# Performance work log

Measured on AMD Instinct MI355X. Metric: run time of the kernel, lower is better.

## Reference

```python
import jax, jax.numpy as jnp
import numpy as np

B, T, E, H = 2, 2048, 1024, 16


def setup_inputs() -> dict:
    key = jax.random.key(0)
    ks = jax.random.split(key, 6)
    s = lambda k, shape: jax.random.normal(k, shape, dtype=jnp.float32) * 0.02
    return {
        "x": jax.random.normal(ks[0], (B, T, E), dtype=jnp.float32),
        "ln1_g": jnp.ones((E,), jnp.float32),
        "ln1_b": jnp.zeros((E,), jnp.float32),
        "attn_w": s(ks[1], (E, 3 * E)),
        "attn_b": jnp.zeros((3 * E,), jnp.float32),
        "proj_w": s(ks[2], (E, E)),
        "proj_b": jnp.zeros((E,), jnp.float32),
        "ln2_g": jnp.ones((E,), jnp.float32),
        "ln2_b": jnp.zeros((E,), jnp.float32),
        "mlp_w1": s(ks[3], (E, 4 * E)),
        "mlp_b1": jnp.zeros((4 * E,), jnp.float32),
        "mlp_w2": s(ks[4], (4 * E, E)),
        "mlp_b2": jnp.zeros((E,), jnp.float32),
        "w_att": jnp.ones((1,), jnp.float32),
        "w_mlp": jnp.ones((1,), jnp.float32),
    }


def _ln(x, g, b, eps=1e-5):
    m = x.mean(-1, keepdims=True)
    v = ((x - m) ** 2).mean(-1, keepdims=True)
    return (x - m) * jax.lax.rsqrt(v + eps) * g + b


def reference(x, ln1_g, ln1_b, attn_w, attn_b, proj_w, proj_b,
              ln2_g, ln2_b, mlp_w1, mlp_b1, mlp_w2, mlp_b2, w_att, w_mlp):
    Bx, Tx, Ex = x.shape
    hd = Ex // H
    # --- self-attention on ln_1(x) ---
    qkv = _ln(x, ln1_g, ln1_b) @ attn_w + attn_b          # [B,T,3E]
    q, k, v = jnp.split(qkv, 3, axis=-1)
    q = q.reshape(Bx, Tx, H, hd)
    k = k.reshape(Bx, Tx, H, hd)
    v = v.reshape(Bx, Tx, H, hd)
    att = jnp.einsum('bthd,bshd->bhts', q, k) * (1.0 / np.sqrt(hd))  # [B,H,T,T]
    causal = jnp.tril(jnp.ones((Tx, Tx), dtype=bool))
    att = jnp.where(causal, att, -jnp.inf)
    att = jax.nn.softmax(att, axis=-1)
    y = jnp.einsum('bhts,bshd->bthd', att, v).reshape(Bx, Tx, Ex)
    y = y @ proj_w + proj_b
    x = x * w_att + y
    # --- MLP on ln_2(x) ---
    h = _ln(x, ln2_g, ln2_b) @ mlp_w1 + mlp_b1
    h = jax.nn.gelu(h, approximate=False)
    x = x * w_mlp + (h @ mlp_w2 + mlp_b2)
    return x
```

## Files before the change

### kernel.cpp

```cpp
#include <hip/hip_runtime.h>
#include <math.h>

typedef __bf16 bf16;
typedef bf16 bf16x8 __attribute__((ext_vector_type(8)));
typedef bf16 bf16x4 __attribute__((ext_vector_type(4)));
typedef float f32x4 __attribute__((ext_vector_type(4)));

#define MFMA(a, b, c) __builtin_amdgcn_mfma_f32_16x16x32_bf16((a), (b), (c), 0, 0, 0)

#define GLOAD_LDS16(gp, lp)                                                        \
  __builtin_amdgcn_global_load_lds((const __attribute__((address_space(1))) void*)(gp), \
                                   (__attribute__((address_space(3))) void*)(lp), 16, 0, 0)

static const size_t E_WT_ATTN = 0;
static const size_t E_WT_PROJ = 3145728;
static const size_t E_WT_MLP1 = 4194304;
static const size_t E_WT_MLP2 = 8388608;
static const size_t E_LN1     = 12582912;
static const size_t E_QKV     = 16777216;
static const size_t E_VT      = 37748736;
static const size_t E_Y       = 41943040;
static const size_t E_LN2     = 46137344;
static const size_t E_H       = 50331648;
static const size_t BYTE_X2    = 134217728;
static const size_t BYTE_OPART = 150994944;
static const size_t BYTE_ML    = 184549376;
static const size_t BYTE_GPART = 185597952;
static const size_t TOTAL_BYTES = 252706816;

__device__ __align__(4096) unsigned char g_buf[TOTAL_BYTES];

__global__ __launch_bounds__(256) void transpose_all(const float* __restrict__ aw,
                                                     const float* __restrict__ pw,
                                                     const float* __restrict__ m1,
                                                     const float* __restrict__ m2,
                                                     bf16* __restrict__ o_a,
                                                     bf16* __restrict__ o_p,
                                                     bf16* __restrict__ o_m1,
                                                     bf16* __restrict__ o_m2) {
  __shared__ float tile[32][33];
  int bid = blockIdx.x;
  const float* in;
  bf16* out;
  int K, N, tix;
  if (bid < 3072) { in = aw; out = o_a; K = 1024; N = 3072; tix = bid; }
  else if (bid < 4096) { in = pw; out = o_p; K = 1024; N = 1024; tix = bid - 3072; }
  else if (bid < 8192) { in = m1; out = o_m1; K = 1024; N = 4096; tix = bid - 4096; }
  else { in = m2; out = o_m2; K = 4096; N = 1024; tix = bid - 8192; }
  int ntx = N >> 5;
  int bx = tix % ntx, by = tix / ntx;
  int tx = threadIdx.x, ty = threadIdx.y;
#pragma unroll
  for (int i = ty; i < 32; i += 8)
    tile[i][tx] = in[(size_t)(by * 32 + i) * N + bx * 32 + tx];
  __syncthreads();
#pragma unroll
  for (int i = ty; i < 32; i += 8)
    out[(size_t)(bx * 32 + i) * K + by * 32 + tx] = (bf16)tile[tx][i];
}

__global__ __launch_bounds__(256) void ln_bf16(const float* __restrict__ x,
                                               const float* __restrict__ g,
                                               const float* __restrict__ b,
                                               bf16* __restrict__ out) {
  int row = blockIdx.x, tid = threadIdx.x;
  const float* xr = x + ((size_t)row << 10);
  float4 v = *(const float4*)(xr + tid * 4);
  float s = v.x + v.y + v.z + v.w;
  float ss = v.x * v.x + v.y * v.y + v.z * v.z + v.w * v.w;
#pragma unroll
  for (int off = 32; off >= 1; off >>= 1) {
    s += __shfl_down(s, off);
    ss += __shfl_down(ss, off);
  }
  __shared__ float sh[8];
  int wid = tid >> 6;
  if ((tid & 63) == 0) { sh[wid] = s; sh[wid + 4] = ss; }
  __syncthreads();
  float ts = sh[0] + sh[1] + sh[2] + sh[3];
  float tss = sh[4] + sh[5] + sh[6] + sh[7];
  float mean = ts * (1.0f / 1024.0f);
  float var = tss * (1.0f / 1024.0f) - mean * mean;
  float inv = rsqrtf(var + 1e-5f);
  float4 gg = *(const float4*)(g + tid * 4);
  float4 bb = *(const float4*)(b + tid * 4);
  bf16x4 o;
  o[0] = (bf16)((v.x - mean) * inv * gg.x + bb.x);
  o[1] = (bf16)((v.y - mean) * inv * gg.y + bb.y);
  o[2] = (bf16)((v.z - mean) * inv * gg.z + bb.z);
  o[3] = (bf16)((v.w - mean) * inv * gg.w + bb.w);
  *(bf16x4*)(out + ((size_t)row << 10) + tid * 4) = o;
}

template <int EPI>
__global__ __launch_bounds__(512, 2) void gemm256(const bf16* __restrict__ A,
                                                  const bf16* __restrict__ Bt,
                                                  const float* __restrict__ bias,
                                                  bf16* __restrict__ outb,
                                                  float* __restrict__ outf,
                                                  int M, int N, int K, int Kseg) {
  __shared__ __align__(16) bf16 As[2][16384];
  __shared__ __align__(16) bf16 Bs[2][16384];
  int tid = threadIdx.x;
  int nwg = gridDim.x * gridDim.y;
  int bid = blockIdx.y * gridDim.x + blockIdx.x;
  int id2 = ((nwg & 7) == 0) ? ((bid & 7) * (nwg >> 3) + (bid >> 3)) : bid;
  int bx = id2 % gridDim.x, by = id2 / gridDim.x;
  int lane = tid & 63, wid = tid >> 6;
  int wr = wid >> 2, wc = wid & 3;
  int g = lane >> 4, lr = lane & 15;
  f32x4 acc[8][4];
#pragma unroll
  for (int m = 0; m < 8; ++m)
#pragma unroll
    for (int n = 0; n < 4; ++n) acc[m][n] = (f32x4){0.f, 0.f, 0.f, 0.f};
  const bf16* Ab = A + (size_t)by * 256 * K;
  const bf16* Bb = Bt + (size_t)bx * 256 * K;
  int rbase = tid >> 3;
  int srccol = (((tid & 7) ^ (rbase & 7)) << 3);
  const bf16* Asrc = Ab + (size_t)rbase * K + srccol;
  const bf16* Bsrc = Bb + (size_t)rbase * K + srccol;
#define G256_STAGE(buf, k0)                                                \
  {                                                                        \
    _Pragma("unroll") for (int q = 0; q < 4; ++q) {                        \
      GLOAD_LDS16(Asrc + (size_t)(q * 64) * K + (k0), &As[buf][tid * 8 + q * 4096]); \
      GLOAD_LDS16(Bsrc + (size_t)(q * 64) * K + (k0), &Bs[buf][tid * 8 + q * 4096]); \
    }                                                                      \
  }
  int kbeg = blockIdx.z * Kseg;
  int NT = Kseg >> 6;
  G256_STAGE(0, kbeg);
  if (NT > 1) {
    G256_STAGE(1, kbeg + 64);
    asm volatile("s_waitcnt vmcnt(8)" ::: "memory");
  } else {
    asm volatile("s_waitcnt vmcnt(0)" ::: "memory");
  }
  __builtin_amdgcn_sched_barrier(0);
  __builtin_amdgcn_s_barrier();
  int c = 0;
  for (int t = 0; t < NT; ++t) {
    bf16x8 a0[8], b0[4], a1[8], b1[4];
#pragma unroll
    for (int m = 0; m < 8; ++m) {
      int row = wr * 128 + m * 16 + lr;
      a0[m] = *(const bf16x8*)&As[c][row * 64 + ((g ^ (row & 7)) << 3)];
      a1[m] = *(const bf16x8*)&As[c][row * 64 + (((4 + g) ^ (row & 7)) << 3)];
    }
#pragma unroll
    for (int n = 0; n < 4; ++n) {
      int row = wc * 64 + n * 16 + lr;
      b0[n] = *(const bf16x8*)&Bs[c][row * 64 + ((g ^ (row & 7)) << 3)];
      b1[n] = *(const bf16x8*)&Bs[c][row * 64 + (((4 + g) ^ (row & 7)) << 3)];
    }
    __builtin_amdgcn_s_setprio(1);
#pragma unroll
    for (int m = 0; m < 8; ++m)
#pragma unroll
      for (int n = 0; n < 4; ++n) acc[m][n] = MFMA(a0[m], b0[n], acc[m][n]);
    __builtin_amdgcn_s_setprio(0);
    asm volatile("s_waitcnt lgkmcnt(0)" ::: "memory");
    __builtin_amdgcn_sched_barrier(0);
    __builtin_amdgcn_s_barrier();
    if (t + 2 < NT) G256_STAGE(c, kbeg + (t + 2) * 64);
    __builtin_amdgcn_s_setprio(1);
#pragma unroll
    for (int m = 0; m < 8; ++m)
#pragma unroll
      for (int n = 0; n < 4; ++n) acc[m][n] = MFMA(a1[m], b1[n], acc[m][n]);
    __builtin_amdgcn_s_setprio(0);
    if (t + 2 < NT) {
      asm volatile("s_waitcnt vmcnt(8)" ::: "memory");
    } else if (t + 1 < NT) {
      asm volatile("s_waitcnt vmcnt(0)" ::: "memory");
    }
    __builtin_amdgcn_sched_barrier(0);
    __builtin_amdgcn_s_barrier();
    c ^= 1;
  }
#undef G256_STAGE
  if (EPI == 3) {
    float* po = outf + (size_t)blockIdx.z * M * N;
#pragma unroll
    for (int m = 0; m < 8; ++m) {
#pragma unroll
      for (int n = 0; n < 4; ++n) {
        int rg0 = by * 256 + wr * 128 + m * 16 + g * 4;
        int cg = bx * 256 + wc * 64 + n * 16 + lr;
#pragma unroll
        for (int j = 0; j < 4; ++j) po[(size_t)(rg0 + j) * N + cg] = acc[m][n][j];
      }
    }
  } else {
#pragma unroll
    for (int m = 0; m < 8; ++m) {
#pragma unroll
      for (int n = 0; n < 4; ++n) {
        int rg0 = by * 256 + wr * 128 + m * 16 + g * 4;
        int cg = bx * 256 + wc * 64 + n * 16 + lr;
        float bv = bias[cg];
#pragma unroll
        for (int j = 0; j < 4; ++j) {
          float v = acc[m][n][j] + bv;
          size_t idx = (size_t)(rg0 + j) * N + cg;
          if (EPI == 0)
            outb[idx] = (bf16)v;
          else {
            float u = 0.7978845608f * (v + 0.044715f * v * v * v);
            float e = exp2f(u * 2.885390082f);
            float th = 1.0f - 2.0f / (e + 1.0f);
            outb[idx] = (bf16)(0.5f * v * (1.0f + th));
          }
        }
      }
    }
  }
}

__global__ __launch_bounds__(256) void gemm_bt3(const bf16* __restrict__ A,
                                                const bf16* __restrict__ Bt,
                                                float* __restrict__ outf,
                                                int M, int N, int K, int Kseg) {
  __shared__ __align__(16) bf16 As[128 * 32];
  __shared__ __align__(16) bf16 Bs[128 * 32];
  int bx = blockIdx.x, by = blockIdx.y;
  int tid = threadIdx.x;
  int lane = tid & 63, wid = tid >> 6;
  int wr = wid >> 1, wc = wid & 1;
  int g = lane >> 4, lr = lane & 15;
  f32x4 acc[4][4];
#pragma unroll
  for (int m = 0; m < 4; ++m)
#pragma unroll
    for (int n = 0; n < 4; ++n) acc[m][n] = (f32x4){0.f, 0.f, 0.f, 0.f};
  const bf16* Ab = A + (size_t)by * 128 * K;
  const bf16* Bb = Bt + (size_t)bx * 128 * K;
  int srow = tid >> 2;
  int sk8 = (tid & 3) * 8;
  const bf16* Ap0 = Ab + (size_t)srow * K + sk8;
  const bf16* Ap1 = Ab + (size_t)(srow + 64) * K + sk8;
  const bf16* Bp0 = Bb + (size_t)srow * K + sk8;
  const bf16* Bp1 = Bb + (size_t)(srow + 64) * K + sk8;
  bf16* lA0 = As + tid * 8;
  bf16* lA1 = As + 2048 + tid * 8;
  bf16* lB0 = Bs + tid * 8;
  bf16* lB1 = Bs + 2048 + tid * 8;
  int kbeg = blockIdx.z * Kseg;
  int kend = kbeg + Kseg;
  for (int k0 = kbeg; k0 < kend; k0 += 32) {
    GLOAD_LDS16(Ap0 + k0, lA0);
    GLOAD_LDS16(Ap1 + k0, lA1);
    GLOAD_LDS16(Bp0 + k0, lB0);
    GLOAD_LDS16(Bp1 + k0, lB1);
    __syncthreads();
    bf16x8 af[4], bfv[4];
#pragma unroll
    for (int m = 0; m < 4; ++m) af[m] = *(const bf16x8*)(As + (wr * 64 + m * 16 + lr) * 32 + g * 8);
#pragma unroll
    for (int n = 0; n < 4; ++n) bfv[n] = *(const bf16x8*)(Bs + (wc * 64 + n * 16 + lr) * 32 + g * 8);
#pragma unroll
    for (int m = 0; m < 4; ++m)
#pragma unroll
      for (int n = 0; n < 4; ++n) acc[m][n] = MFMA(af[m], bfv[n], acc[m][n]);
    __syncthreads();
  }
  float* po = outf + (size_t)blockIdx.z * M * N;
#pragma unroll
  for (int m = 0; m < 4; ++m) {
#pragma unroll
    for (int n = 0; n < 4; ++n) {
      int rg0 = by * 128 + wr * 64 + m * 16 + g * 4;
      int cg = bx * 128 + wc * 64 + n * 16 + lr;
#pragma unroll
      for (int j = 0; j < 4; ++j) po[(size_t)(rg0 + j) * N + cg] = acc[m][n][j];
    }
  }
}

template <int SK>
__global__ __launch_bounds__(256) void reduce_add(const float* __restrict__ part,
                                                  const float* __restrict__ bias,
                                                  const float* __restrict__ res,
                                                  const float* __restrict__ wsc,
                                                  float* __restrict__ out, int MN, int N) {
  size_t i = ((size_t)blockIdx.x * 256 + threadIdx.x) * 4;
  float4 a = *(const float4*)(part + i);
#pragma unroll
  for (int s = 1; s < SK; ++s) {
    float4 b = *(const float4*)(part + (size_t)s * MN + i);
    a.x += b.x; a.y += b.y; a.z += b.z; a.w += b.w;
  }
  int col = (int)(i & (size_t)(N - 1));
  float4 bv = *(const float4*)(bias + col);
  float4 rv = *(const float4*)(res + i);
  float w = wsc[0];
  float4 o;
  o.x = rv.x * w + a.x + bv.x;
  o.y = rv.y * w + a.y + bv.y;
  o.z = rv.z * w + a.z + bv.z;
  o.w = rv.w * w + a.w + bv.w;
  *(float4*)(out + i) = o;
}

__global__ __launch_bounds__(256) void reduce_ln(const float* __restrict__ part,
                                                 const float* __restrict__ bias,
                                                 const float* __restrict__ res,
                                                 const float* __restrict__ wsc,
                                                 const float* __restrict__ lng,
                                                 const float* __restrict__ lnb,
                                                 float* __restrict__ x2out,
                                                 bf16* __restrict__ lnout) {
  int row = blockIdx.x, tid = threadIdx.x;
  size_t i = ((size_t)row << 10) + tid * 4;
  float4 a = *(const float4*)(part + i);
  float4 b2 = *(const float4*)(part + 4194304 + i);
  float4 rv = *(const float4*)(res + i);
  float4 bv = *(const float4*)(bias + tid * 4);
  float w = wsc[0];
  float4 o;
  o.x = rv.x * w + a.x + b2.x + bv.x;
  o.y = rv.y * w + a.y + b2.y + bv.y;
  o.z = rv.z * w + a.z + b2.z + bv.z;
  o.w = rv.w * w + a.w + b2.w + bv.w;
  *(float4*)(x2out + i) = o;
  float s = o.x + o.y + o.z + o.w;
  float ss = o.x * o.x + o.y * o.y + o.z * o.z + o.w * o.w;
#pragma unroll
  for (int off = 32; off >= 1; off >>= 1) {
    s += __shfl_down(s, off);
    ss += __shfl_down(ss, off);
  }
  __shared__ float sh[8];
  int wid = tid >> 6;
  if ((tid & 63) == 0) { sh[wid] = s; sh[wid + 4] = ss; }
  __syncthreads();
  float ts = sh[0] + sh[1] + sh[2] + sh[3];
  float tss = sh[4] + sh[5] + sh[6] + sh[7];
  float mean = ts * (1.0f / 1024.0f);
  float var = tss * (1.0f / 1024.0f) - mean * mean;
  float inv = rsqrtf(var + 1e-5f);
  float4 gg = *(const float4*)(lng + tid * 4);
  float4 bb = *(const float4*)(lnb + tid * 4);
  bf16x4 ov;
  ov[0] = (bf16)((o.x - mean) * inv * gg.x + bb.x);
  ov[1] = (bf16)((o.y - mean) * inv * gg.y + bb.y);
  ov[2] = (bf16)((o.z - mean) * inv * gg.z + bb.z);
  ov[3] = (bf16)((o.w - mean) * inv * gg.w + bb.w);
  *(bf16x4*)(lnout + ((size_t)row << 10) + tid * 4) = ov;
}

__global__ __launch_bounds__(256) void split_v_t(const bf16* __restrict__ qkv,
                                                 bf16* __restrict__ vT) {
  int t0 = blockIdx.x * 32;
  int bh = blockIdx.y;
  int b = bh >> 4, h = bh & 15;
  __shared__ bf16 tile[32][72];
  int tid = threadIdx.x;
  int d = tid & 63, tl0 = tid >> 6;
#pragma unroll
  for (int p = 0; p < 8; ++p) {
    int tl = p * 4 + tl0;
    tile[tl][d] = qkv[((size_t)(b * 2048 + t0 + tl)) * 3072 + 2048 + h * 64 + d];
  }
  __syncthreads();
  int tl = tid & 31, dq = tid >> 5;
#pragma unroll
  for (int p = 0; p < 8; ++p) {
    int dd = p * 8 + dq;
    vT[((size_t)(bh * 64 + dd)) * 2048 + t0 + tl] = tile[tl][dd];
  }
}

__global__ __launch_bounds__(256) void attn_fwd(const bf16* __restrict__ qkv,
                                                const bf16* __restrict__ vT,
                                                float* __restrict__ o_part,
                                                float* __restrict__ ml_part) {
  __shared__ __align__(16) bf16 Ks[2][4096];
  __shared__ __align__(16) bf16 Vs[2][4096];
  __shared__ bf16 P[4][16][136];
  int id = blockIdx.x;
  int bh = id & 31;
  int seg = (id >> 5) & 1;
  int qi = ((id >> 6) + bh) & 31;
  int tid = threadIdx.x, wid = tid >> 6, lane = tid & 63;
  int g = lane >> 4, lr = lane & 15;
  int b = bh >> 4, h = bh & 15;
  int nk = qi + 1;
  int n0 = (nk + 1) >> 1;
  int kt0 = seg ? n0 : 0;
  int kt1 = seg ? nk : n0;
  int nt = kt1 - kt0;
  int qrow = qi * 64 + wid * 16 + lr;
  const bf16* Qr = qkv + ((size_t)(b * 2048 + qrow)) * 3072 + h * 64;
  const float beta = 0.18033688f;
  bf16x8 qf[2];
  qf[0] = *(const bf16x8*)(Qr + g * 8);
  qf[1] = *(const bf16x8*)(Qr + 32 + g * 8);
#pragma unroll
  for (int kk = 0; kk < 2; ++kk)
#pragma unroll
    for (int e = 0; e < 8; ++e) qf[kk][e] = (bf16)((float)qf[kk][e] * beta);
  int r0 = tid >> 3, cs0 = ((tid & 7) ^ (r0 & 7)) << 3;
  int c1i = tid + 256;
  int r1 = c1i >> 3, cs1 = ((c1i & 7) ^ (r1 & 7)) << 3;
  const bf16* sK0 = qkv + ((size_t)(b * 2048 + r0)) * 3072 + 1024 + h * 64 + cs0;
  const bf16* sK1 = qkv + ((size_t)(b * 2048 + r1)) * 3072 + 1024 + h * 64 + cs1;
  const bf16* sV0 = vT + (size_t)bh * 131072 + (size_t)r0 * 2048 + cs0;
  const bf16* sV1 = vT + (size_t)bh * 131072 + (size_t)r1 * 2048 + cs1;
  bf16* dK0 = &Ks[0][0] + tid * 8;
  bf16* dK1 = &Ks[0][0] + 2048 + tid * 8;
  bf16* dV0 = &Vs[0][0] + tid * 8;
  bf16* dV1 = &Vs[0][0] + 2048 + tid * 8;
#define STAGE_K(bufsel, ktv)                              \
  {                                                       \
    size_t kadv = (size_t)(ktv) * (64 * 3072);            \
    int bo = (bufsel) * 4096;                             \
    GLOAD_LDS16(sK0 + kadv, dK0 + bo);                    \
    GLOAD_LDS16(sK1 + kadv, dK1 + bo);                    \
  }
#define STAGE_V(bufsel, ktv)                              \
  {                                                       \
    size_t vadv = (size_t)(ktv) * 64;                     \
    int bo = (bufsel) * 4096;                             \
    GLOAD_LDS16(sV0 + vadv, dV0 + bo);                    \
    GLOAD_LDS16(sV1 + vadv, dV1 + bo);                    \
  }
  f32x4 o[4];
#pragma unroll
  for (int n = 0; n < 4; ++n) o[n] = (f32x4){0.f, 0.f, 0.f, 0.f};
  float m = -3e38f, l = 0.f;
  int sw = lr & 7;
  int sb = (lane & 48) | (g << 2);
  if (nt > 0) {
    STAGE_K(0, kt0);
    STAGE_K(1, kt0 + 1);
    STAGE_V(0, kt0);
    STAGE_V(1, kt0 + 1);
  }
  int kt = kt0;
  for (; kt + 2 <= kt1; kt += 2) {
    asm volatile("s_waitcnt vmcnt(4)" ::: "memory");
    __builtin_amdgcn_sched_barrier(0);
    __builtin_amdgcn_s_barrier();
    f32x4 s0[4], s1[4];
#pragma unroll
    for (int n = 0; n < 4; ++n) { s0[n] = (f32x4){0.f,0.f,0.f,0.f}; s1[n] = (f32x4){0.f,0.f,0.f,0.f}; }
    __builtin_amdgcn_s_setprio(1);
#pragma unroll
    for (int kk = 0; kk < 2; ++kk) {
#pragma unroll
      for (int n = 0; n < 4; ++n) {
        int off = ((n * 16 + lr) << 6) + ((((kk << 2) + g) ^ sw) << 3);
        bf16x8 kf0 = *(const bf16x8*)(&Ks[0][0] + off);
        s0[n] = MFMA(kf0, qf[kk], s0[n]);
        bf16x8 kf1 = *(const bf16x8*)(&Ks[1][0] + off);
        s1[n] = MFMA(kf1, qf[kk], s1[n]);
      }
    }
    __builtin_amdgcn_s_setprio(0);
    asm volatile("s_waitcnt lgkmcnt(0)" ::: "memory");
    __builtin_amdgcn_sched_barrier(0);
    __builtin_amdgcn_s_barrier();
    STAGE_K(0, kt + 2);
    STAGE_K(1, kt + 3);
    if (kt + 1 == qi) {
      int kc0 = (kt + 1) * 64 + g * 4;
#pragma unroll
      for (int n = 0; n < 4; ++n)
#pragma unroll
        for (int j = 0; j < 4; ++j)
          if ((kc0 + n * 16 + j) > qrow) s1[n][j] = -3e38f;
    }
    float mx = s0[0][0];
#pragma unroll
    for (int n = 0; n < 4; ++n)
#pragma unroll
      for (int j = 0; j < 4; ++j) { mx = fmaxf(mx, s0[n][j]); mx = fmaxf(mx, s1[n][j]); }
    mx = fmaxf(mx, __shfl_xor(mx, 16));
    mx = fmaxf(mx, __shfl_xor(mx, 32));
    bool defer = __all(mx <= m + 11.5416f);
    float mn = m, al = 0.f;
    if (!defer) {
      mn = fmaxf(m, mx);
      al = exp2f(m - mn);
      m = mn;
    }
    float rs = 0.f;
    bf16x4 pw0[4], pw1[4];
#pragma unroll
    for (int n = 0; n < 4; ++n)
#pragma unroll
      for (int j = 0; j < 4; ++j) {
        float p0 = exp2f(s0[n][j] - mn);
        float p1 = exp2f(s1[n][j] - mn);
        rs += p0 + p1;
        pw0[n][j] = (bf16)p0;
        pw1[n][j] = (bf16)p1;
      }
    rs += __shfl_xor(rs, 16);
    rs += __shfl_xor(rs, 32);
    if (defer) {
      l += rs;
    } else {
      l = l * al + rs;
      float alj[4];
#pragma unroll
      for (int j = 0; j < 4; ++j) alj[j] = __shfl(al, sb + j);
#pragma unroll
      for (int n = 0; n < 4; ++n)
#pragma unroll
        for (int j = 0; j < 4; ++j) o[n][j] *= alj[j];
    }
#pragma unroll
    for (int n = 0; n < 4; ++n) {
      *(bf16x4*)&P[wid][lr][n * 16 + g * 4] = pw0[n];
      *(bf16x4*)&P[wid][lr][64 + n * 16 + g * 4] = pw1[n];
    }
    asm volatile("s_waitcnt vmcnt(4)" ::: "memory");
    __builtin_amdgcn_sched_barrier(0);
    __builtin_amdgcn_s_barrier();
    __builtin_amdgcn_s_setprio(1);
#pragma unroll
    for (int kk = 0; kk < 2; ++kk) {
      bf16x8 pf0 = *(const bf16x8*)&P[wid][lr][kk * 32 + g * 8];
      bf16x8 pf1 = *(const bf16x8*)&P[wid][lr][64 + kk * 32 + g * 8];
#pragma unroll
      for (int n = 0; n < 4; ++n) {
        int off = ((n * 16 + lr) << 6) + ((((kk << 2) + g) ^ sw) << 3);
        bf16x8 vf0 = *(const bf16x8*)(&Vs[0][0] + off);
        o[n] = MFMA(pf0, vf0, o[n]);
        bf16x8 vf1 = *(const bf16x8*)(&Vs[1][0] + off);
        o[n] = MFMA(pf1, vf1, o[n]);
      }
    }
    __builtin_amdgcn_s_setprio(0);
    asm volatile("s_waitcnt lgkmcnt(0)" ::: "memory");
    __builtin_amdgcn_sched_barrier(0);
    __builtin_amdgcn_s_barrier();
    STAGE_V(0, kt + 2);
    STAGE_V(1, kt + 3);
  }
  if (kt < kt1) {
    int lb = (kt - kt0) & 1;
    asm volatile("s_waitcnt vmcnt(4)" ::: "memory");
    __builtin_amdgcn_sched_barrier(0);
    __builtin_amdgcn_s_barrier();
    f32x4 s0[4];
#pragma unroll
    for (int n = 0; n < 4; ++n) s0[n] = (f32x4){0.f,0.f,0.f,0.f};
    __builtin_amdgcn_s_setprio(1);
#pragma unroll
    for (int kk = 0; kk < 2; ++kk) {
#pragma unroll
      for (int n = 0; n < 4; ++n) {
        int off = ((n * 16 + lr) << 6) + ((((kk << 2) + g) ^ sw) << 3);
        bf16x8 kf = *(const bf16x8*)(&Ks[lb][0] + off);
        s0[n] = MFMA(kf, qf[kk], s0[n]);
      }
    }
    __builtin_amdgcn_s_setprio(0);
    if (kt == qi) {
      int kc0 = kt * 64 + g * 4;
#pragma unroll
      for (int n = 0; n < 4; ++n)
#pragma unroll
        for (int j = 0; j < 4; ++j)
          if ((kc0 + n * 16 + j) > qrow) s0[n][j] = -3e38f;
    }
    float mx = s0[0][0];
#pragma unroll
    for (int n = 0; n < 4; ++n)
#pragma unroll
      for (int j = 0; j < 4; ++j) mx = fmaxf(mx, s0[n][j]);
    mx = fmaxf(mx, __shfl_xor(mx, 16));
    mx = fmaxf(mx, __shfl_xor(mx, 32));
    bool defer = __all(mx <= m + 11.5416f);
    float mn = m, al = 0.f;
    if (!defer) {
      mn = fmaxf(m, mx);
      al = exp2f(m - mn);
      m = mn;
    }
    float rs = 0.f;
    bf16x4 pw0[4];
#pragma unroll
    for (int n = 0; n < 4; ++n)
#pragma unroll
      for (int j = 0; j < 4; ++j) {
        float p = exp2f(s0[n][j] - mn);
        rs += p;
        pw0[n][j] = (bf16)p;
      }
    rs += __shfl_xor(rs, 16);
    rs += __shfl_xor(rs, 32);
    if (defer) {
      l += rs;
    } else {
      l = l * al + rs;
      float alj[4];
#pragma unroll
      for (int j = 0; j < 4; ++j) alj[j] = __shfl(al, sb + j);
#pragma unroll
      for (int n = 0; n < 4; ++n)
#pragma unroll
        for (int j = 0; j < 4; ++j) o[n][j] *= alj[j];
    }
#pragma unroll
    for (int n = 0; n < 4; ++n) *(bf16x4*)&P[wid][lr][n * 16 + g * 4] = pw0[n];
    asm volatile("s_waitcnt vmcnt(0)" ::: "memory");
    __builtin_amdgcn_sched_barrier(0);
    __builtin_amdgcn_s_barrier();
    __builtin_amdgcn_s_setprio(1);
#pragma unroll
    for (int kk = 0; kk < 2; ++kk) {
      bf16x8 pf = *(const bf16x8*)&P[wid][lr][kk * 32 + g * 8];
#pragma unroll
      for (int n = 0; n < 4; ++n) {
        int off = ((n * 16 + lr) << 6) + ((((kk << 2) + g) ^ sw) << 3);
        bf16x8 vf = *(const bf16x8*)(&Vs[lb][0] + off);
        o[n] = MFMA(pf, vf, o[n]);
      }
    }
    __builtin_amdgcn_s_setprio(0);
  }
  float* ob = o_part + (size_t)id * 4096;
#pragma unroll
  for (int n = 0; n < 4; ++n)
#pragma unroll
    for (int j = 0; j < 4; ++j)
      ob[(size_t)(wid * 16 + g * 4 + j) * 64 + n * 16 + lr] = o[n][j];
  if (lane < 16) {
    ml_part[(size_t)id * 128 + (wid * 16 + lane) * 2] = m;
    ml_part[(size_t)id * 128 + (wid * 16 + lane) * 2 + 1] = l;
  }
#undef STAGE_K
#undef STAGE_V
}

__global__ __launch_bounds__(256) void attn_combine(const float* __restrict__ o_part,
                                                    const float* __restrict__ ml_part,
                                                    bf16* __restrict__ y) {
  int c = blockIdx.x;
  int bh = c & 31, qi = c >> 5;
  int b = bh >> 4, h = bh & 15;
  int qraw = (qi - bh) & 31;
  size_t id0 = (size_t)bh + ((size_t)qraw << 6);
  size_t id1 = id0 + 32;
  int t = threadIdx.x;
  int r = t >> 2, cq = (t & 3) << 4;
  float m1 = ml_part[id0 * 128 + r * 2], l1 = ml_part[id0 * 128 + r * 2 + 1];
  float m2 = ml_part[id1 * 128 + r * 2], l2 = ml_part[id1 * 128 + r * 2 + 1];
  float mm = fmaxf(m1, m2);
  float w1 = exp2f(m1 - mm), w2 = exp2f(m2 - mm);
  float inv = 1.0f / (l1 * w1 + l2 * w2);
  const float* p1 = o_part + id0 * 4096 + r * 64 + cq;
  const float* p2 = o_part + id1 * 4096 + r * 64 + cq;
  bf16* yp = y + ((size_t)(b * 2048 + qi * 64 + r)) * 1024 + h * 64 + cq;
#pragma unroll
  for (int u = 0; u < 4; ++u) {
    float4 a = *(const float4*)(p1 + u * 4);
    float4 bq = *(const float4*)(p2 + u * 4);
    bf16x4 ov;
    ov[0] = (bf16)((a.x * w1 + bq.x * w2) * inv);
    ov[1] = (bf16)((a.y * w1 + bq.y * w2) * inv);
    ov[2] = (bf16)((a.z * w1 + bq.z * w2) * inv);
    ov[3] = (bf16)((a.w * w1 + bq.w * w2) * inv);
    *(bf16x4*)(yp + u * 4) = ov;
  }
}

extern "C" void kernel_launch(void* const* d_in, const int* in_sizes, int n_in,
                              void* d_out, int out_size, void* d_ws, size_t ws_size,
                              hipStream_t stream) {
  const float* x = (const float*)d_in[0];
  const float* ln1_g = (const float*)d_in[1];
  const float* ln1_b = (const float*)d_in[2];
  const float* attn_w = (const float*)d_in[3];
  const float* attn_b = (const float*)d_in[4];
  const float* proj_w = (const float*)d_in[5];
  const float* proj_b = (const float*)d_in[6];
  const float* ln2_g = (const float*)d_in[7];
  const float* ln2_b = (const float*)d_in[8];
  const float* mlp_w1 = (const float*)d_in[9];
  const float* mlp_b1 = (const float*)d_in[10];
  const float* mlp_w2 = (const float*)d_in[11];
  const float* mlp_b2 = (const float*)d_in[12];
  const float* w_att = (const float*)d_in[13];
  const float* w_mlp = (const float*)d_in[14];
  float* out = (float*)d_out;

  unsigned char* base = nullptr;
  if (ws_size >= TOTAL_BYTES) {
    base = (unsigned char*)d_ws;
  } else {
    hipGetSymbolAddress((void**)&base, HIP_SYMBOL(g_buf));
  }
  bf16* bb = (bf16*)base;
  bf16* wt_attn = bb + E_WT_ATTN;
  bf16* wt_proj = bb + E_WT_PROJ;
  bf16* wt_mlp1 = bb + E_WT_MLP1;
  bf16* wt_mlp2 = bb + E_WT_MLP2;
  bf16* ln1o = bb + E_LN1;
  bf16* qkv = bb + E_QKV;
  bf16* vTb = bb + E_VT;
  bf16* yb = bb + E_Y;
  bf16* ln2o = bb + E_LN2;
  bf16* hb = bb + E_H;
  float* x2 = (float*)(base + BYTE_X2);
  float* o_part = (float*)(base + BYTE_OPART);
  float* ml_part = (float*)(base + BYTE_ML);
  float* gpart = (float*)(base + BYTE_GPART);

  transpose_all<<<12288, dim3(32, 8), 0, stream>>>(attn_w, proj_w, mlp_w1, mlp_w2,
                                                   wt_attn, wt_proj, wt_mlp1, wt_mlp2);

  ln_bf16<<<4096, 256, 0, stream>>>(x, ln1_g, ln1_b, ln1o);

  gemm256<0><<<dim3(12, 16, 1), 512, 0, stream>>>(ln1o, wt_attn, attn_b, qkv, nullptr,
                                                  4096, 3072, 1024, 1024);

  split_v_t<<<dim3(64, 32), 256, 0, stream>>>(qkv, vTb);

  attn_fwd<<<2048, 256, 0, stream>>>(qkv, vTb, o_part, ml_part);
  attn_combine<<<1024, 256, 0, stream>>>(o_part, ml_part, yb);

  gemm_bt3<<<dim3(8, 32, 2), 256, 0, stream>>>(yb, wt_proj, gpart, 4096, 1024, 1024, 512);
  reduce_ln<<<4096, 256, 0, stream>>>(gpart, proj_b, x, w_att, ln2_g, ln2_b, x2, ln2o);

  gemm256<1><<<dim3(16, 16, 1), 512, 0, stream>>>(ln2o, wt_mlp1, mlp_b1, hb, nullptr,
                                                  4096, 4096, 1024, 1024);

  gemm256<3><<<dim3(4, 16, 4), 512, 0, stream>>>(hb, wt_mlp2, nullptr, nullptr, gpart,
                                                 4096, 1024, 4096, 1024);
  reduce_add<4><<<4096, 256, 0, stream>>>(gpart, mlp_b2, x2, w_mlp, out, 4194304, 1024);
}
```

Baseline: 369.3 us.

## Split attention KV range into four segments and store partials in bf16

```diff
diff --git a/kernel.cpp b/kernel.cpp
--- a/kernel.cpp
+++ b/kernel.cpp
@@ -25,8 +25,8 @@
 static const size_t BYTE_X2    = 134217728;
 static const size_t BYTE_OPART = 150994944;
 static const size_t BYTE_ML    = 184549376;
-static const size_t BYTE_GPART = 185597952;
-static const size_t TOTAL_BYTES = 252706816;
+static const size_t BYTE_GPART = 186646528;
+static const size_t TOTAL_BYTES = 253755392;
 
 __device__ __align__(4096) unsigned char g_buf[TOTAL_BYTES];
 
@@ -373,22 +373,21 @@
 
 __global__ __launch_bounds__(256) void attn_fwd(const bf16* __restrict__ qkv,
                                                 const bf16* __restrict__ vT,
-                                                float* __restrict__ o_part,
+                                                bf16* __restrict__ o_part,
                                                 float* __restrict__ ml_part) {
   __shared__ __align__(16) bf16 Ks[2][4096];
   __shared__ __align__(16) bf16 Vs[2][4096];
   __shared__ bf16 P[4][16][136];
   int id = blockIdx.x;
   int bh = id & 31;
-  int seg = (id >> 5) & 1;
-  int qi = ((id >> 6) + bh) & 31;
+  int seg = (id >> 5) & 3;
+  int qi = ((id >> 7) + bh) & 31;
   int tid = threadIdx.x, wid = tid >> 6, lane = tid & 63;
   int g = lane >> 4, lr = lane & 15;
   int b = bh >> 4, h = bh & 15;
   int nk = qi + 1;
-  int n0 = (nk + 1) >> 1;
-  int kt0 = seg ? n0 : 0;
-  int kt1 = seg ? nk : n0;
+  int kt0 = (nk * seg) >> 2;
+  int kt1 = (nk * (seg + 1)) >> 2;
   int nt = kt1 - kt0;
   int qrow = qi * 64 + wid * 16 + lr;
   const bf16* Qr = qkv + ((size_t)(b * 2048 + qrow)) * 3072 + h * 64;
@@ -623,12 +622,12 @@
     }
     __builtin_amdgcn_s_setprio(0);
   }
-  float* ob = o_part + (size_t)id * 4096;
+  bf16* ob = o_part + (size_t)id * 4096;
 #pragma unroll
   for (int n = 0; n < 4; ++n)
 #pragma unroll
     for (int j = 0; j < 4; ++j)
-      ob[(size_t)(wid * 16 + g * 4 + j) * 64 + n * 16 + lr] = o[n][j];
+      ob[(size_t)(wid * 16 + g * 4 + j) * 64 + n * 16 + lr] = (bf16)o[n][j];
   if (lane < 16) {
     ml_part[(size_t)id * 128 + (wid * 16 + lane) * 2] = m;
     ml_part[(size_t)id * 128 + (wid * 16 + lane) * 2 + 1] = l;
@@ -637,36 +636,55 @@
 #undef STAGE_V
 }
 
-__global__ __launch_bounds__(256) void attn_combine(const float* __restrict__ o_part,
+__global__ __launch_bounds__(256) void attn_combine(const bf16* __restrict__ o_part,
                                                     const float* __restrict__ ml_part,
                                                     bf16* __restrict__ y) {
   int c = blockIdx.x;
   int bh = c & 31, qi = c >> 5;
   int b = bh >> 4, h = bh & 15;
   int qraw = (qi - bh) & 31;
-  size_t id0 = (size_t)bh + ((size_t)qraw << 6);
-  size_t id1 = id0 + 32;
+  size_t idbase = (size_t)bh + ((size_t)qraw << 7);
   int t = threadIdx.x;
   int r = t >> 2, cq = (t & 3) << 4;
-  float m1 = ml_part[id0 * 128 + r * 2], l1 = ml_part[id0 * 128 + r * 2 + 1];
-  float m2 = ml_part[id1 * 128 + r * 2], l2 = ml_part[id1 * 128 + r * 2 + 1];
-  float mm = fmaxf(m1, m2);
-  float w1 = exp2f(m1 - mm), w2 = exp2f(m2 - mm);
-  float inv = 1.0f / (l1 * w1 + l2 * w2);
-  const float* p1 = o_part + id0 * 4096 + r * 64 + cq;
-  const float* p2 = o_part + id1 * 4096 + r * 64 + cq;
+  float mv[4], lv[4];
+#pragma unroll
+  for (int s = 0; s < 4; ++s) {
+    size_t ids = idbase + ((size_t)s << 5);
+    mv[s] = ml_part[ids * 128 + r * 2];
+    lv[s] = ml_part[ids * 128 + r * 2 + 1];
+  }
+  float mm = fmaxf(fmaxf(mv[0], mv[1]), fmaxf(mv[2], mv[3]));
+  float ws[4], denom = 0.f;
+#pragma unroll
+  for (int s = 0; s < 4; ++s) {
+    ws[s] = exp2f(mv[s] - mm);
+    denom += lv[s] * ws[s];
+  }
+  float inv = 1.0f / denom;
+  float accv[16];
+#pragma unroll
+  for (int u = 0; u < 16; ++u) accv[u] = 0.f;
+#pragma unroll
+  for (int s = 0; s < 4; ++s) {
+    const bf16* ps = o_part + (idbase + ((size_t)s << 5)) * 4096 + r * 64 + cq;
+    bf16x8 v0 = *(const bf16x8*)ps;
+    bf16x8 v1 = *(const bf16x8*)(ps + 8);
+    float w = ws[s];
+#pragma unroll
+    for (int u = 0; u < 8; ++u) {
+      accv[u] += (float)v0[u] * w;
+      accv[8 + u] += (float)v1[u] * w;
+    }
+  }
   bf16* yp = y + ((size_t)(b * 2048 + qi * 64 + r)) * 1024 + h * 64 + cq;
-#pragma unroll
-  for (int u = 0; u < 4; ++u) {
-    float4 a = *(const float4*)(p1 + u * 4);
-    float4 bq = *(const float4*)(p2 + u * 4);
-    bf16x4 ov;
-    ov[0] = (bf16)((a.x * w1 + bq.x * w2) * inv);
-    ov[1] = (bf16)((a.y * w1 + bq.y * w2) * inv);
-    ov[2] = (bf16)((a.z * w1 + bq.z * w2) * inv);
-    ov[3] = (bf16)((a.w * w1 + bq.w * w2) * inv);
-    *(bf16x4*)(yp + u * 4) = ov;
-  }
+  bf16x8 ov0, ov1;
+#pragma unroll
+  for (int u = 0; u < 8; ++u) {
+    ov0[u] = (bf16)(accv[u] * inv);
+    ov1[u] = (bf16)(accv[8 + u] * inv);
+  }
+  *(bf16x8*)yp = ov0;
+  *(bf16x8*)(yp + 8) = ov1;
 }
 
 extern "C" void kernel_launch(void* const* d_in, const int* in_sizes, int n_in,
@@ -707,7 +725,7 @@
   bf16* ln2o = bb + E_LN2;
   bf16* hb = bb + E_H;
   float* x2 = (float*)(base + BYTE_X2);
-  float* o_part = (float*)(base + BYTE_OPART);
+  bf16* o_part = (bf16*)(base + BYTE_OPART);
   float* ml_part = (float*)(base + BYTE_ML);
   float* gpart = (float*)(base + BYTE_GPART);
 
@@ -721,7 +739,7 @@
 
   split_v_t<<<dim3(64, 32), 256, 0, stream>>>(qkv, vTb);
 
-  attn_fwd<<<2048, 256, 0, stream>>>(qkv, vTb, o_part, ml_part);
+  attn_fwd<<<4096, 256, 0, stream>>>(qkv, vTb, o_part, ml_part);
   attn_combine<<<1024, 256, 0, stream>>>(o_part, ml_part, yb);
 
   gemm_bt3<<<dim3(8, 32, 2), 256, 0, stream>>>(yb, wt_proj, gpart, 4096, 1024, 1024, 512);
```

New measurement: 386.2 us. +4.6%, slower.
